# Kernel optimization log

Measured on AMD Instinct MI355X. Metric: run time of the kernel, lower is better.

The kernel has to match this reference:

```python
import jax, jax.numpy as jnp
import numpy as np

WINDOW = 5  # window_size from init


def _avg_pool3d(x, k):
    # Matches F.avg_pool3d(kernel=k, stride=1, padding=k//2,
    # count_include_pad=True): windowed sum with zero padding / k^3.
    pad = k // 2
    s = jax.lax.reduce_window(
        x, 0.0, jax.lax.add,
        window_dimensions=(1, 1, k, k, k),
        window_strides=(1, 1, 1, 1, 1),
        padding=[(0, 0), (0, 0), (pad, pad), (pad, pad), (pad, pad)],
    )
    return s / float(k ** 3)


def setup_inputs() -> dict:
    key = jax.random.key(0)
    k1, k2 = jax.random.split(key)
    shape = (2, 1, 160, 192, 192)  # [B, C, D, H, W]
    source = jax.random.normal(k1, shape, dtype=jnp.float32)
    target = jax.random.normal(k2, shape, dtype=jnp.float32)
    return {"source": source, "target": target}


def reference(source, target):
    conv = lambda x: _avg_pool3d(x, WINDOW)
    src_mean = conv(source)
    tgt_mean = conv(target)
    src_var = conv(source * source) - src_mean * src_mean
    tgt_var = conv(target * target) - tgt_mean * tgt_mean
    cross = conv(source * target) - src_mean * tgt_mean
    lncc = cross * cross / (src_var * tgt_var + 1e-5)
    loss = 1.0 - jnp.mean(lncc)
    return jnp.nan_to_num(loss, nan=1.0, posinf=1.0, neginf=1.0)
```

## Files before the change

### kernel.cpp

```cpp
#include <hip/hip_runtime.h>
#include <math.h>

#define W_ 192
#define H_ 192
#define D_ 160
#define B_ 2
#define CHUNK 40
#define TILE 16
#define HALO 20
#define NTOT 11796480.0f

struct Q { float ss, tt, s2, t2, st; };

__global__ __launch_bounds__(256) void lncc_main(const float* __restrict__ src,
                                                 const float* __restrict__ tgt,
                                                 float* __restrict__ acc) {
    __shared__ float2 tileP[HALO][HALO];
    __shared__ float  wsum[4];

    const int tx  = threadIdx.x, ty = threadIdx.y;
    const int tid = ty * TILE + tx;
    const int bz  = blockIdx.z;
    const int b   = bz >> 2;
    const int z0  = (bz & 3) * CHUNK;
    const int bx0 = blockIdx.x * TILE - 2;
    const int by0 = blockIdx.y * TILE - 2;

    Q r0 = {}, r1 = {}, r2 = {}, r3 = {}, r4 = {};
    float lsum = 0.0f;

    for (int zp = z0 - 2; zp < z0 + CHUNK + 2; ++zp) {
        Q cur = {};
        if (zp >= 0 && zp < D_) {
            __syncthreads();
            const size_t planeBase = (size_t)(b * D_ + zp) * (size_t)(H_ * W_);
            for (int f = tid; f < HALO * HALO; f += TILE * TILE) {
                int r  = f / HALO;
                int c  = f - r * HALO;
                int gy = by0 + r, gx = bx0 + c;
                float sv = 0.0f, tv = 0.0f;
                if (gx >= 0 && gx < W_ && gy >= 0 && gy < H_) {
                    size_t idx = planeBase + (size_t)gy * W_ + (size_t)gx;
                    sv = src[idx];
                    tv = tgt[idx];
                }
                tileP[r][c] = make_float2(sv, tv);
            }
            __syncthreads();
            #pragma unroll
            for (int dy = 0; dy < 5; ++dy) {
                #pragma unroll
                for (int dx = 0; dx < 5; ++dx) {
                    float2 v = tileP[ty + dy][tx + dx];
                    cur.ss += v.x;
                    cur.tt += v.y;
                    cur.s2 = fmaf(v.x, v.x, cur.s2);
                    cur.t2 = fmaf(v.y, v.y, cur.t2);
                    cur.st = fmaf(v.x, v.y, cur.st);
                }
            }
        }
        r0 = r1; r1 = r2; r2 = r3; r3 = r4; r4 = cur;

        if (zp >= z0 + 2) {
            const float inv = 1.0f / 125.0f;
            float ssum  = r0.ss + r1.ss + r2.ss + r3.ss + r4.ss;
            float tsum  = r0.tt + r1.tt + r2.tt + r3.tt + r4.tt;
            float s2sum = r0.s2 + r1.s2 + r2.s2 + r3.s2 + r4.s2;
            float t2sum = r0.t2 + r1.t2 + r2.t2 + r3.t2 + r4.t2;
            float stsum = r0.st + r1.st + r2.st + r3.st + r4.st;
            float ms = ssum * inv, mt = tsum * inv;
            float vs = s2sum * inv - ms * ms;
            float vt = t2sum * inv - mt * mt;
            float cr = stsum * inv - ms * mt;
            lsum += cr * cr / (vs * vt + 1e-5f);
        }
    }

    #pragma unroll
    for (int off = 32; off > 0; off >>= 1)
        lsum += __shfl_down(lsum, off, 64);
    if ((tid & 63) == 0) wsum[tid >> 6] = lsum;
    __syncthreads();
    if (tid == 0) {
        float t = wsum[0] + wsum[1] + wsum[2] + wsum[3];
        atomicAdd(acc, t);
    }
}

__global__ void lncc_zero(float* acc) { *acc = 0.0f; }

__global__ void lncc_finalize(const float* __restrict__ acc, float* __restrict__ out) {
    float loss = 1.0f - (*acc) * (1.0f / NTOT);
    if (isnan(loss) || isinf(loss)) loss = 1.0f;
    *out = loss;
}

extern "C" void kernel_launch(void* const* d_in, const int* in_sizes, int n_in,
                              void* d_out, int out_size, void* d_ws, size_t ws_size,
                              hipStream_t stream) {
    const float* src = (const float*)d_in[0];
    const float* tgt = (const float*)d_in[1];
    float* out = (float*)d_out;
    float* acc = (float*)d_ws;

    lncc_zero<<<dim3(1), dim3(1), 0, stream>>>(acc);

    dim3 grid(W_ / TILE, H_ / TILE, B_ * (D_ / CHUNK));
    dim3 block(TILE, TILE, 1);
    lncc_main<<<grid, block, 0, stream>>>(src, tgt, acc);

    lncc_finalize<<<dim3(1), dim3(1), 0, stream>>>(acc, out);
}
```

Before: 183.6 us.

## Separable box sums with double-buffered float2 tiles and partial-sum reduction

Replaces the 25-tap per-plane stencil with a separable scheme. Row sums over x are computed once per pair of columns into shared arrays, then summed over y, then kept as a running sum over z. Each thread now handles two x outputs, loads use float2 with a double-buffered raw tile so the next plane's global loads overlap compute, and the division becomes a hardware reciprocal. Chunks are shorter to give more blocks, and the atomic accumulate plus zero kernel is replaced by per-block partials summed in a parallel finalize kernel. The trade-offs are extra shared-memory traffic and barriers, a larger z halo overhead per chunk, and slightly different floating-point rounding from the running sums and approximate reciprocal.

```diff
diff --git a/kernel.cpp b/kernel.cpp
--- a/kernel.cpp
+++ b/kernel.cpp
@@ -5,95 +5,182 @@
 #define H_ 192
 #define D_ 160
 #define B_ 2
-#define CHUNK 40
-#define TILE 16
-#define HALO 20
+#define XT 32
+#define YT 16
+#define HX 36
+#define HY 20
+#define CHUNK 10
+#define PLANES (CHUNK + 4)
+#define GXD 6
+#define GYD 12
+#define GZD 32
+#define NBLK (GXD * GYD * GZD)
 #define NTOT 11796480.0f
 
-struct Q { float ss, tt, s2, t2, st; };
+struct Q2 { float2 s, t, a, b, c; };
+
+__device__ __forceinline__ float2 f2add(float2 u, float2 v) { return make_float2(u.x + v.x, u.y + v.y); }
+__device__ __forceinline__ float2 f2sub(float2 u, float2 v) { return make_float2(u.x - v.x, u.y - v.y); }
 
 __global__ __launch_bounds__(256) void lncc_main(const float* __restrict__ src,
                                                  const float* __restrict__ tgt,
-                                                 float* __restrict__ acc) {
-    __shared__ float2 tileP[HALO][HALO];
-    __shared__ float  wsum[4];
+                                                 float* __restrict__ partial) {
+    __shared__ float4 raw[2][HY][19];
+    __shared__ float2 rsS [HY][17];
+    __shared__ float2 rsT [HY][17];
+    __shared__ float2 rsS2[HY][17];
+    __shared__ float2 rsT2[HY][17];
+    __shared__ float2 rsST[HY][17];
+    __shared__ float wsum[4];
 
     const int tx  = threadIdx.x, ty = threadIdx.y;
-    const int tid = ty * TILE + tx;
+    const int tid = ty * 16 + tx;
     const int bz  = blockIdx.z;
-    const int b   = bz >> 2;
-    const int z0  = (bz & 3) * CHUNK;
-    const int bx0 = blockIdx.x * TILE - 2;
-    const int by0 = blockIdx.y * TILE - 2;
+    const int b   = bz >> 4;
+    const int z0  = (bz & 15) * CHUNK;
+    const int bx0 = blockIdx.x * XT - 2;
+    const int by0 = blockIdx.y * YT - 2;
 
-    Q r0 = {}, r1 = {}, r2 = {}, r3 = {}, r4 = {};
-    float lsum = 0.0f;
+    const int  r0s = tid / 18,          c0s = tid - r0s * 18;
+    const int  s1  = 256 + tid;
+    const int  r1s = s1 / 18,           c1s = s1 - r1s * 18;
+    const bool has2 = (tid < 104);
 
-    for (int zp = z0 - 2; zp < z0 + CHUNK + 2; ++zp) {
-        Q cur = {};
-        if (zp >= 0 && zp < D_) {
-            __syncthreads();
-            const size_t planeBase = (size_t)(b * D_ + zp) * (size_t)(H_ * W_);
-            for (int f = tid; f < HALO * HALO; f += TILE * TILE) {
-                int r  = f / HALO;
-                int c  = f - r * HALO;
-                int gy = by0 + r, gx = bx0 + c;
-                float sv = 0.0f, tv = 0.0f;
-                if (gx >= 0 && gx < W_ && gy >= 0 && gy < H_) {
-                    size_t idx = planeBase + (size_t)gy * W_ + (size_t)gx;
-                    sv = src[idx];
-                    tv = tgt[idx];
-                }
-                tileP[r][c] = make_float2(sv, tv);
-            }
-            __syncthreads();
+    auto load_slot = [&](int r, int c, int zp, float2& vS, float2& vT) {
+        vS = make_float2(0.f, 0.f); vT = make_float2(0.f, 0.f);
+        const int gx = bx0 + 2 * c, gy = by0 + r;
+        if ((unsigned)zp < (unsigned)D_ && (unsigned)gy < (unsigned)H_ &&
+            (unsigned)gx < (unsigned)W_) {
+            const size_t off = (size_t)(b * D_ + zp) * (size_t)(H_ * W_)
+                             + (size_t)gy * W_ + (size_t)gx;
+            vS = *(const float2*)(src + off);
+            vT = *(const float2*)(tgt + off);
+        }
+    };
+    auto store_slot = [&](int bf, int r, int c, float2 vS, float2 vT) {
+        raw[bf][r][c] = make_float4(vS.x, vT.x, vS.y, vT.y);
+    };
+
+    auto do_pair = [&](int p, int bf) {
+        const int r = p >> 4, px = p & 15;
+        float4 A = raw[bf][r][px];
+        float4 Bv = raw[bf][r][px + 1];
+        float4 C = raw[bf][r][px + 2];
+        float s0 = A.x,  t0 = A.y,  sx1 = A.z,  tx1 = A.w;
+        float s2 = Bv.x, t2 = Bv.y, s3 = Bv.z,  t3 = Bv.w;
+        float s4 = C.x,  t4 = C.y,  s5 = C.z,   t5 = C.w;
+        float S0 = s0 + sx1 + s2 + s3 + s4;
+        float T0 = t0 + tx1 + t2 + t3 + t4;
+        float A0 = fmaf(s4, s4, fmaf(s3, s3, fmaf(s2, s2, fmaf(sx1, sx1, s0 * s0))));
+        float B0 = fmaf(t4, t4, fmaf(t3, t3, fmaf(t2, t2, fmaf(tx1, tx1, t0 * t0))));
+        float C0 = fmaf(s4, t4, fmaf(s3, t3, fmaf(s2, t2, fmaf(sx1, tx1, s0 * t0))));
+        float S1 = S0 - s0 + s5;
+        float T1 = T0 - t0 + t5;
+        float A1 = fmaf(s5, s5, fmaf(-s0, s0, A0));
+        float B1 = fmaf(t5, t5, fmaf(-t0, t0, B0));
+        float C1 = fmaf(s5, t5, fmaf(-s0, t0, C0));
+        rsS [r][px] = make_float2(S0, S1);
+        rsT [r][px] = make_float2(T0, T1);
+        rsS2[r][px] = make_float2(A0, A1);
+        rsT2[r][px] = make_float2(B0, B1);
+        rsST[r][px] = make_float2(C0, C1);
+    };
+
+    Q2 q0 = {}, q1 = {}, q2 = {}, q3 = {}, q4 = {};
+    Q2 zs = {};
+    float2 lsum = make_float2(0.f, 0.f);
+
+    {
+        float2 aS, aT, bS, bT;
+        load_slot(r0s, c0s, z0 - 2, aS, aT);
+        if (has2) load_slot(r1s, c1s, z0 - 2, bS, bT);
+        store_slot(0, r0s, c0s, aS, aT);
+        if (has2) store_slot(0, r1s, c1s, bS, bT);
+    }
+
+    for (int i = 0; i < PLANES; ++i) {
+        const int buf = i & 1;
+        __syncthreads();
+        float2 aS, aT, bS, bT;
+        const bool haveNext = (i + 1 < PLANES);
+        if (haveNext) {
+            load_slot(r0s, c0s, z0 - 1 + i, aS, aT);
+            if (has2) load_slot(r1s, c1s, z0 - 1 + i, bS, bT);
+        }
+        do_pair(tid, buf);
+        if (tid < 64) do_pair(256 + tid, buf);
+        __syncthreads();
+        {
+            float2 yS = make_float2(0.f, 0.f), yT = yS, yA = yS, yB = yS, yC = yS;
             #pragma unroll
             for (int dy = 0; dy < 5; ++dy) {
-                #pragma unroll
-                for (int dx = 0; dx < 5; ++dx) {
-                    float2 v = tileP[ty + dy][tx + dx];
-                    cur.ss += v.x;
-                    cur.tt += v.y;
-                    cur.s2 = fmaf(v.x, v.x, cur.s2);
-                    cur.t2 = fmaf(v.y, v.y, cur.t2);
-                    cur.st = fmaf(v.x, v.y, cur.st);
+                yS = f2add(yS, rsS [ty + dy][tx]);
+                yT = f2add(yT, rsT [ty + dy][tx]);
+                yA = f2add(yA, rsS2[ty + dy][tx]);
+                yB = f2add(yB, rsT2[ty + dy][tx]);
+                yC = f2add(yC, rsST[ty + dy][tx]);
+            }
+            zs.s = f2add(zs.s, f2sub(yS, q0.s));
+            zs.t = f2add(zs.t, f2sub(yT, q0.t));
+            zs.a = f2add(zs.a, f2sub(yA, q0.a));
+            zs.b = f2add(zs.b, f2sub(yB, q0.b));
+            zs.c = f2add(zs.c, f2sub(yC, q0.c));
+            q0 = q1; q1 = q2; q2 = q3; q3 = q4;
+            q4.s = yS; q4.t = yT; q4.a = yA; q4.b = yB; q4.c = yC;
+            if (i >= 4) {
+                const float inv = 1.0f / 125.0f;
+                {
+                    float ms = zs.s.x * inv, mt = zs.t.x * inv;
+                    float vs = fmaf(-ms, ms, zs.a.x * inv);
+                    float vt = fmaf(-mt, mt, zs.b.x * inv);
+                    float cr = fmaf(-ms, mt, zs.c.x * inv);
+                    float den = fmaf(vs, vt, 1e-5f);
+                    lsum.x = fmaf(cr * cr, __builtin_amdgcn_rcpf(den), lsum.x);
+                }
+                {
+                    float ms = zs.s.y * inv, mt = zs.t.y * inv;
+                    float vs = fmaf(-ms, ms, zs.a.y * inv);
+                    float vt = fmaf(-mt, mt, zs.b.y * inv);
+                    float cr = fmaf(-ms, mt, zs.c.y * inv);
+                    float den = fmaf(vs, vt, 1e-5f);
+                    lsum.y = fmaf(cr * cr, __builtin_amdgcn_rcpf(den), lsum.y);
                 }
             }
         }
-        r0 = r1; r1 = r2; r2 = r3; r3 = r4; r4 = cur;
-
-        if (zp >= z0 + 2) {
-            const float inv = 1.0f / 125.0f;
-            float ssum  = r0.ss + r1.ss + r2.ss + r3.ss + r4.ss;
-            float tsum  = r0.tt + r1.tt + r2.tt + r3.tt + r4.tt;
-            float s2sum = r0.s2 + r1.s2 + r2.s2 + r3.s2 + r4.s2;
-            float t2sum = r0.t2 + r1.t2 + r2.t2 + r3.t2 + r4.t2;
-            float stsum = r0.st + r1.st + r2.st + r3.st + r4.st;
-            float ms = ssum * inv, mt = tsum * inv;
-            float vs = s2sum * inv - ms * ms;
-            float vt = t2sum * inv - mt * mt;
-            float cr = stsum * inv - ms * mt;
-            lsum += cr * cr / (vs * vt + 1e-5f);
+        if (haveNext) {
+            store_slot(buf ^ 1, r0s, c0s, aS, aT);
+            if (has2) store_slot(buf ^ 1, r1s, c1s, bS, bT);
         }
     }
 
+    float ls = lsum.x + lsum.y;
     #pragma unroll
     for (int off = 32; off > 0; off >>= 1)
-        lsum += __shfl_down(lsum, off, 64);
-    if ((tid & 63) == 0) wsum[tid >> 6] = lsum;
+        ls += __shfl_down(ls, off, 64);
+    if ((tid & 63) == 0) wsum[tid >> 6] = ls;
     __syncthreads();
     if (tid == 0) {
-        float t = wsum[0] + wsum[1] + wsum[2] + wsum[3];
-        atomicAdd(acc, t);
+        const int bid = (blockIdx.z * GYD + blockIdx.y) * GXD + blockIdx.x;
+        partial[bid] = wsum[0] + wsum[1] + wsum[2] + wsum[3];
     }
 }
 
-__global__ void lncc_zero(float* acc) { *acc = 0.0f; }
-
-__global__ void lncc_finalize(const float* __restrict__ acc, float* __restrict__ out) {
-    float loss = 1.0f - (*acc) * (1.0f / NTOT);
-    if (isnan(loss) || isinf(loss)) loss = 1.0f;
-    *out = loss;
+__global__ __launch_bounds__(256) void lncc_finalize(const float* __restrict__ partial,
+                                                     float* __restrict__ out) {
+    __shared__ float ws[4];
+    const int t = threadIdx.x;
+    float s = 0.0f;
+    for (int i = t; i < NBLK; i += 256) s += partial[i];
+    #pragma unroll
+    for (int off = 32; off > 0; off >>= 1) s += __shfl_down(s, off, 64);
+    if ((t & 63) == 0) ws[t >> 6] = s;
+    __syncthreads();
+    if (t == 0) {
+        float tot = ws[0] + ws[1] + ws[2] + ws[3];
+        float loss = 1.0f - tot * (1.0f / NTOT);
+        if (isnan(loss) || isinf(loss)) loss = 1.0f;
+        *out = loss;
+    }
 }
 
 extern "C" void kernel_launch(void* const* d_in, const int* in_sizes, int n_in,
@@ -102,13 +189,10 @@
     const float* src = (const float*)d_in[0];
     const float* tgt = (const float*)d_in[1];
     float* out = (float*)d_out;
-    float* acc = (float*)d_ws;
+    float* partial = (float*)d_ws;
 
-    lncc_zero<<<dim3(1), dim3(1), 0, stream>>>(acc);
-
-    dim3 grid(W_ / TILE, H_ / TILE, B_ * (D_ / CHUNK));
-    dim3 block(TILE, TILE, 1);
-    lncc_main<<<grid, block, 0, stream>>>(src, tgt, acc);
-
-    lncc_finalize<<<dim3(1), dim3(1), 0, stream>>>(acc, out);
+    dim3 grid(GXD, GYD, GZD);
+    dim3 block(16, 16, 1);
+    lncc_main<<<grid, block, 0, stream>>>(src, tgt, partial);
+    lncc_finalize<<<dim3(1), dim3(256), 0, stream>>>(partial, out);
 }
```

Result: faster. 174.9 us (-4.7%).

## Rewrite LNCC as separable register box filter with wave shuffles

Applied to the files above, without the earlier changes.

Replaces the shared-memory 5x5 stencil per plane with a separable scheme. Each lane loads a float2 column pair and sums five rows directly from global memory, keeps a running z-window sum in registers, and takes the x-window sum with wave shuffles. Atomics are replaced by per-block partials plus a reduction kernel, the zero kernel is dropped, and division becomes a fast reciprocal. The costs are redundant global row loads across warps (which lean on the caches), idle lanes (16 of 64 per wave are masked off), more z-halo overhead from the smaller chunk, and slightly lower precision from the approximate reciprocal.

```diff
diff --git a/kernel.cpp b/kernel.cpp
--- a/kernel.cpp
+++ b/kernel.cpp
@@ -5,95 +5,158 @@
 #define H_ 192
 #define D_ 160
 #define B_ 2
-#define CHUNK 40
-#define TILE 16
-#define HALO 20
+#define XTILE 96
+#define CHUNK 20
+#define STEPS (CHUNK + 4)
+#define NYB 48
+#define NBLK (NYB * 2 * 8 * 2)
 #define NTOT 11796480.0f
-
-struct Q { float ss, tt, s2, t2, st; };
 
 __global__ __launch_bounds__(256) void lncc_main(const float* __restrict__ src,
                                                  const float* __restrict__ tgt,
-                                                 float* __restrict__ acc) {
-    __shared__ float2 tileP[HALO][HALO];
-    __shared__ float  wsum[4];
+                                                 float* __restrict__ partial) {
+    __shared__ float wsum[4];
 
-    const int tx  = threadIdx.x, ty = threadIdx.y;
-    const int tid = ty * TILE + tx;
-    const int bz  = blockIdx.z;
-    const int b   = bz >> 2;
-    const int z0  = (bz & 3) * CHUNK;
-    const int bx0 = blockIdx.x * TILE - 2;
-    const int by0 = blockIdx.y * TILE - 2;
+    const int tid = threadIdx.x;
+    const int l   = tid & 63;
+    const int w   = tid >> 6;
+    const int bid = blockIdx.x;
+    const int y   = (bid % NYB) * 4 + w;
+    int rest      = bid / NYB;
+    const int xt  = rest & 1;  rest >>= 1;
+    const int zc  = rest & 7;
+    const int b   = rest >> 3;
+    const int z0  = zc * CHUNK;
 
-    Q r0 = {}, r1 = {}, r2 = {}, r3 = {}, r4 = {};
-    float lsum = 0.0f;
+    const int   x0  = xt * XTILE - 2 + 2 * l;
+    const int   xc  = min(max(x0, 0), W_ - 2);
+    const float mx0 = (x0     >= 0 && x0     < W_) ? 1.f : 0.f;
+    const float mx1 = (x0 + 1 >= 0 && x0 + 1 < W_) ? 1.f : 0.f;
+    const float mvalid = (l < 48) ? 1.f : 0.f;
 
-    for (int zp = z0 - 2; zp < z0 + CHUNK + 2; ++zp) {
-        Q cur = {};
-        if (zp >= 0 && zp < D_) {
-            __syncthreads();
+    float2 q0S={0,0},q0T={0,0},q0A={0,0},q0B={0,0},q0C={0,0};
+    float2 q1S={0,0},q1T={0,0},q1A={0,0},q1B={0,0},q1C={0,0};
+    float2 q2S={0,0},q2T={0,0},q2A={0,0},q2B={0,0},q2C={0,0};
+    float2 q3S={0,0},q3T={0,0},q3A={0,0},q3B={0,0},q3C={0,0};
+    float2 q4S={0,0},q4T={0,0},q4A={0,0},q4B={0,0},q4C={0,0};
+    float2 zS={0,0},zT={0,0},zA={0,0},zB={0,0},zC={0,0};
+    float2 lsum = make_float2(0.f, 0.f);
+
+    const float inv = 1.0f / 125.0f;
+
+    for (int i = 0; i < STEPS; ++i) {
+        const int zp  = z0 - 2 + i;
+        const bool zok = ((unsigned)zp < (unsigned)D_);
+        float2 ysS={0,0}, ysT={0,0}, ysA={0,0}, ysB={0,0}, ysC={0,0};
+        if (zok) {
             const size_t planeBase = (size_t)(b * D_ + zp) * (size_t)(H_ * W_);
-            for (int f = tid; f < HALO * HALO; f += TILE * TILE) {
-                int r  = f / HALO;
-                int c  = f - r * HALO;
-                int gy = by0 + r, gx = bx0 + c;
-                float sv = 0.0f, tv = 0.0f;
-                if (gx >= 0 && gx < W_ && gy >= 0 && gy < H_) {
-                    size_t idx = planeBase + (size_t)gy * W_ + (size_t)gx;
-                    sv = src[idx];
-                    tv = tgt[idx];
-                }
-                tileP[r][c] = make_float2(sv, tv);
-            }
-            __syncthreads();
             #pragma unroll
-            for (int dy = 0; dy < 5; ++dy) {
-                #pragma unroll
-                for (int dx = 0; dx < 5; ++dx) {
-                    float2 v = tileP[ty + dy][tx + dx];
-                    cur.ss += v.x;
-                    cur.tt += v.y;
-                    cur.s2 = fmaf(v.x, v.x, cur.s2);
-                    cur.t2 = fmaf(v.y, v.y, cur.t2);
-                    cur.st = fmaf(v.x, v.y, cur.st);
+            for (int r = 0; r < 5; ++r) {
+                const int ry = y - 2 + r;
+                if ((unsigned)ry < (unsigned)H_) {
+                    const float* rowS = src + planeBase + (size_t)ry * W_;
+                    const float* rowT = tgt + planeBase + (size_t)ry * W_;
+                    const float2 sv = *(const float2*)(rowS + xc);
+                    const float2 tv = *(const float2*)(rowT + xc);
+                    ysS.x += sv.x;  ysS.y += sv.y;
+                    ysT.x += tv.x;  ysT.y += tv.y;
+                    ysA.x = fmaf(sv.x, sv.x, ysA.x);  ysA.y = fmaf(sv.y, sv.y, ysA.y);
+                    ysB.x = fmaf(tv.x, tv.x, ysB.x);  ysB.y = fmaf(tv.y, tv.y, ysB.y);
+                    ysC.x = fmaf(sv.x, tv.x, ysC.x);  ysC.y = fmaf(sv.y, tv.y, ysC.y);
                 }
             }
+            ysS.x *= mx0; ysS.y *= mx1;
+            ysT.x *= mx0; ysT.y *= mx1;
+            ysA.x *= mx0; ysA.y *= mx1;
+            ysB.x *= mx0; ysB.y *= mx1;
+            ysC.x *= mx0; ysC.y *= mx1;
         }
-        r0 = r1; r1 = r2; r2 = r3; r3 = r4; r4 = cur;
+        zS.x += ysS.x - q0S.x;  zS.y += ysS.y - q0S.y;
+        zT.x += ysT.x - q0T.x;  zT.y += ysT.y - q0T.y;
+        zA.x += ysA.x - q0A.x;  zA.y += ysA.y - q0A.y;
+        zB.x += ysB.x - q0B.x;  zB.y += ysB.y - q0B.y;
+        zC.x += ysC.x - q0C.x;  zC.y += ysC.y - q0C.y;
+        q0S=q1S; q0T=q1T; q0A=q1A; q0B=q1B; q0C=q1C;
+        q1S=q2S; q1T=q2T; q1A=q2A; q1B=q2B; q1C=q2C;
+        q2S=q3S; q2T=q3T; q2A=q3A; q2B=q3B; q2C=q3C;
+        q3S=q4S; q3T=q4T; q3A=q4A; q3B=q4B; q3C=q4C;
+        q4S=ysS; q4T=ysT; q4A=ysA; q4B=ysB; q4C=ysC;
 
-        if (zp >= z0 + 2) {
-            const float inv = 1.0f / 125.0f;
-            float ssum  = r0.ss + r1.ss + r2.ss + r3.ss + r4.ss;
-            float tsum  = r0.tt + r1.tt + r2.tt + r3.tt + r4.tt;
-            float s2sum = r0.s2 + r1.s2 + r2.s2 + r3.s2 + r4.s2;
-            float t2sum = r0.t2 + r1.t2 + r2.t2 + r3.t2 + r4.t2;
-            float stsum = r0.st + r1.st + r2.st + r3.st + r4.st;
-            float ms = ssum * inv, mt = tsum * inv;
-            float vs = s2sum * inv - ms * ms;
-            float vt = t2sum * inv - mt * mt;
-            float cr = stsum * inv - ms * mt;
-            lsum += cr * cr / (vs * vt + 1e-5f);
+        if (i >= 4) {
+            float2 wS, wT, wA, wB, wC;
+            {
+                float n1x = __shfl_down(zS.x, 1), n1y = __shfl_down(zS.y, 1);
+                float n2x = __shfl_down(zS.x, 2), n2y = __shfl_down(zS.y, 2);
+                wS.x = zS.x + zS.y + n1x + n1y + n2x;  wS.y = wS.x - zS.x + n2y;
+            }
+            {
+                float n1x = __shfl_down(zT.x, 1), n1y = __shfl_down(zT.y, 1);
+                float n2x = __shfl_down(zT.x, 2), n2y = __shfl_down(zT.y, 2);
+                wT.x = zT.x + zT.y + n1x + n1y + n2x;  wT.y = wT.x - zT.x + n2y;
+            }
+            {
+                float n1x = __shfl_down(zA.x, 1), n1y = __shfl_down(zA.y, 1);
+                float n2x = __shfl_down(zA.x, 2), n2y = __shfl_down(zA.y, 2);
+                wA.x = zA.x + zA.y + n1x + n1y + n2x;  wA.y = wA.x - zA.x + n2y;
+            }
+            {
+                float n1x = __shfl_down(zB.x, 1), n1y = __shfl_down(zB.y, 1);
+                float n2x = __shfl_down(zB.x, 2), n2y = __shfl_down(zB.y, 2);
+                wB.x = zB.x + zB.y + n1x + n1y + n2x;  wB.y = wB.x - zB.x + n2y;
+            }
+            {
+                float n1x = __shfl_down(zC.x, 1), n1y = __shfl_down(zC.y, 1);
+                float n2x = __shfl_down(zC.x, 2), n2y = __shfl_down(zC.y, 2);
+                wC.x = zC.x + zC.y + n1x + n1y + n2x;  wC.y = wC.x - zC.x + n2y;
+            }
+            {
+                float ms = wS.x * inv, mt = wT.x * inv;
+                float vs = fmaf(-ms, ms, wA.x * inv);
+                float vt = fmaf(-mt, mt, wB.x * inv);
+                float cr = fmaf(-ms, mt, wC.x * inv);
+                float den = fmaf(vs, vt, 1e-5f);
+                float ln0 = cr * cr * __builtin_amdgcn_rcpf(den);
+                lsum.x = fmaf(ln0, mvalid, lsum.x);
+            }
+            {
+                float ms = wS.y * inv, mt = wT.y * inv;
+                float vs = fmaf(-ms, ms, wA.y * inv);
+                float vt = fmaf(-mt, mt, wB.y * inv);
+                float cr = fmaf(-ms, mt, wC.y * inv);
+                float den = fmaf(vs, vt, 1e-5f);
+                float ln1 = cr * cr * __builtin_amdgcn_rcpf(den);
+                lsum.y = fmaf(ln1, mvalid, lsum.y);
+            }
         }
     }
 
+    float ls = lsum.x + lsum.y;
     #pragma unroll
     for (int off = 32; off > 0; off >>= 1)
-        lsum += __shfl_down(lsum, off, 64);
-    if ((tid & 63) == 0) wsum[tid >> 6] = lsum;
+        ls += __shfl_down(ls, off, 64);
+    if (l == 0) wsum[w] = ls;
     __syncthreads();
     if (tid == 0) {
-        float t = wsum[0] + wsum[1] + wsum[2] + wsum[3];
-        atomicAdd(acc, t);
+        partial[bid] = (wsum[0] + wsum[1]) + (wsum[2] + wsum[3]);
     }
 }
 
-__global__ void lncc_zero(float* acc) { *acc = 0.0f; }
-
-__global__ void lncc_finalize(const float* __restrict__ acc, float* __restrict__ out) {
-    float loss = 1.0f - (*acc) * (1.0f / NTOT);
-    if (isnan(loss) || isinf(loss)) loss = 1.0f;
-    *out = loss;
+__global__ __launch_bounds__(256) void lncc_finalize(const float* __restrict__ partial,
+                                                     float* __restrict__ out) {
+    __shared__ float ws[4];
+    const int t = threadIdx.x;
+    float s = 0.0f;
+    for (int i = t; i < NBLK; i += 256) s += partial[i];
+    #pragma unroll
+    for (int off = 32; off > 0; off >>= 1) s += __shfl_down(s, off, 64);
+    if ((t & 63) == 0) ws[t >> 6] = s;
+    __syncthreads();
+    if (t == 0) {
+        float tot = ws[0] + ws[1] + ws[2] + ws[3];
+        float loss = 1.0f - tot * (1.0f / NTOT);
+        if (isnan(loss) || isinf(loss)) loss = 1.0f;
+        *out = loss;
+    }
 }
 
 extern "C" void kernel_launch(void* const* d_in, const int* in_sizes, int n_in,
@@ -102,13 +165,8 @@
     const float* src = (const float*)d_in[0];
     const float* tgt = (const float*)d_in[1];
     float* out = (float*)d_out;
-    float* acc = (float*)d_ws;
+    float* partial = (float*)d_ws;
 
-    lncc_zero<<<dim3(1), dim3(1), 0, stream>>>(acc);
-
-    dim3 grid(W_ / TILE, H_ / TILE, B_ * (D_ / CHUNK));
-    dim3 block(TILE, TILE, 1);
-    lncc_main<<<grid, block, 0, stream>>>(src, tgt, acc);
-
-    lncc_finalize<<<dim3(1), dim3(1), 0, stream>>>(acc, out);
+    lncc_main<<<dim3(NBLK), dim3(256), 0, stream>>>(src, tgt, partial);
+    lncc_finalize<<<dim3(1), dim3(256), 0, stream>>>(partial, out);
 }
```

Result: slower. 254.4 us (+38.6%).
